# Performance work log

Hardware: AMD Instinct MI355X
Metric: run time of the kernel (lower is better)

The kernel has to match this reference:

```python
import jax, jax.numpy as jnp
import numpy as np

N_NODES = 100000
N_EDGES = 1600000
C = 64          # in = hidden = out channels
L = 3           # num_layers
BN_EPS = 1e-5


def setup_inputs() -> dict:
    key = jax.random.key(0)
    ks = jax.random.split(key, 16)
    x = jax.random.normal(ks[0], (N_NODES, C), dtype=jnp.float32)
    edge_index = jax.random.randint(ks[1], (2, N_EDGES), 0, N_NODES, dtype=jnp.int32)
    s = 1.0 / np.sqrt(C)
    # Stacked per-layer parameters (all layers are C->C).
    # Linear weights stored as [in, out] (i.e. torch weight transposed).
    W1 = jax.random.normal(ks[2], (L, C, C), dtype=jnp.float32) * s
    b1 = jnp.zeros((L, C), dtype=jnp.float32)
    g1 = jnp.ones((L, C), dtype=jnp.float32)    # MLP BN1 gamma
    be1 = jnp.zeros((L, C), dtype=jnp.float32)  # MLP BN1 beta
    W2 = jax.random.normal(ks[3], (L, C, C), dtype=jnp.float32) * s
    b2 = jnp.zeros((L, C), dtype=jnp.float32)
    g2 = jnp.ones((L, C), dtype=jnp.float32)
    be2 = jnp.zeros((L, C), dtype=jnp.float32)
    bn_g = jnp.ones((L, C), dtype=jnp.float32)   # outer per-layer BN gamma
    bn_be = jnp.zeros((L, C), dtype=jnp.float32)
    eps = jnp.zeros((L,), dtype=jnp.float32)     # GIN eps per layer
    return {"x": x, "edge_index": edge_index, "eps": eps,
            "W1": W1, "b1": b1, "g1": g1, "be1": be1,
            "W2": W2, "b2": b2, "g2": g2, "be2": be2,
            "bn_g": bn_g, "bn_be": bn_be}


def _bn(h, g, b):
    # Inference-mode BatchNorm1d with running_mean=0, running_var=1.
    return g * (h * (1.0 / np.sqrt(1.0 + BN_EPS))) + b


def reference(x, edge_index, eps, W1, b1, g1, be1, W2, b2, g2, be2, bn_g, bn_be):
    src, dst = edge_index[0], edge_index[1]
    for i in range(L):
        # GIN message passing: gather source features, scatter-add to targets.
        agg = jax.ops.segment_sum(x[src], dst, num_segments=N_NODES)  # [N, C]
        h = (1.0 + eps[i]) * x + agg
        # 2-layer MLP: Linear -> BN -> ReLU, twice.
        h = jax.nn.relu(_bn(h @ W1[i] + b1[i], g1[i], be1[i]))
        h = jax.nn.relu(_bn(h @ W2[i] + b2[i], g2[i], be2[i]))
        # Outer per-layer BatchNorm.
        x = _bn(h, bn_g[i], bn_be[i])
        if i < L - 1:
            x = jax.nn.relu(x)  # dropout is identity in eval mode
    return x
```

## Files before the change

kernel.cpp:

```cpp
#include <hip/hip_runtime.h>
#include <hip/hip_fp16.h>

#define N_NODES 100000
#define N_EDGES 1600000
#define CH 64
#define NLAYERS 3
#define NBUCKC 98
#define SLABC 18432
#define NFINE (NBUCKC*8)
#define SLABF 2560
#define EPB 4096

typedef _Float16 half8 __attribute__((ext_vector_type(8)));
typedef float floatx4 __attribute__((ext_vector_type(4)));

static __device__ __forceinline__ float4 ld4(const float* p){ return *(const float4*)p; }
static __device__ __forceinline__ unsigned pack2(float a, float b){
  __half2 h = __float22half2_rn(make_float2(a, b));
  return *(unsigned*)&h;
}
static __device__ __forceinline__ half8 ldh8(const unsigned short* p){
  uint4 u = *(const uint4*)p;
  return *(half8*)&u;
}

__global__ __launch_bounds__(256) void binit_kernel(int* __restrict__ btail, int* __restrict__ ftail){
  int i = blockIdx.x*256 + threadIdx.x;
  if (i < NBUCKC) btail[i] = i*SLABC;
  if (i < NFINE)  ftail[i] = i*SLABF;
}

__global__ __launch_bounds__(256) void part1_kernel(const int* __restrict__ src, const int* __restrict__ dst,
                                                    int* __restrict__ btail, int* __restrict__ pairs){
  __shared__ int lpos[NBUCKC];
  __shared__ int gb[NBUCKC];
  int tid = threadIdx.x;
  if (tid < NBUCKC) lpos[tid] = 0;
  __syncthreads();
  int base = blockIdx.x * EPB;
  #pragma unroll 4
  for (int k = 0; k < EPB/256; ++k) {
    int e = base + k*256 + tid;
    if (e < N_EDGES) atomicAdd(&lpos[dst[e] >> 10], 1);
  }
  __syncthreads();
  if (tid < NBUCKC) {
    int cc = lpos[tid];
    gb[tid] = cc ? atomicAdd(&btail[tid], cc) : 0;
    lpos[tid] = 0;
  }
  __syncthreads();
  #pragma unroll 4
  for (int k = 0; k < EPB/256; ++k) {
    int e = base + k*256 + tid;
    if (e < N_EDGES) {
      int d = dst[e];
      int bk = d >> 10;
      int p = atomicAdd(&lpos[bk], 1);
      int idx = gb[bk] + p;
      if (idx < (bk+1)*SLABC)
        pairs[idx] = src[e] | ((d & 1023) << 20);
    }
  }
}

__global__ __launch_bounds__(256) void part2_kernel(const int* __restrict__ pairs, const int* __restrict__ btail,
                                                    int* __restrict__ ftail, int* __restrict__ pairs2){
  __shared__ int cnt[8*32];
  __shared__ int scur[8];
  int tid = threadIdx.x;
  int b = blockIdx.x >> 3;
  int sg = blockIdx.x & 7;
  int e0 = b*SLABC;
  int e1 = btail[b]; int emax = e0 + SLABC; if (e1 > emax) e1 = emax;
  int len = e1 - e0;
  int s0 = e0 + (int)(((long)len * sg) >> 3);
  int s1 = e0 + (int)(((long)len * (sg+1)) >> 3);
  cnt[tid] = 0;
  __syncthreads();
  for (int i = s0 + tid; i < s1; i += 256) {
    int p = pairs[i];
    int fk = ((unsigned)p >> 27);
    atomicAdd(&cnt[(fk<<5) + (tid & 31)], 1);
  }
  __syncthreads();
  if (tid < 8) {
    int tot = 0;
    #pragma unroll
    for (int r = 0; r < 32; ++r) tot += cnt[(tid<<5) + r];
    scur[tid] = tot ? atomicAdd(&ftail[(b<<3) + tid], tot) : 0;
  }
  __syncthreads();
  int lane = tid & 63;
  for (int i = s0 + (tid >> 6)*64; i < s1; i += 256) {
    int my = i + lane;
    bool valid = (my < s1);
    int p = valid ? pairs[my] : 0;
    int fk = valid ? (int)((unsigned)p >> 27) : -1;
    #pragma unroll
    for (int j = 0; j < 8; ++j) {
      unsigned long long mask = __ballot(valid && fk == j);
      if (mask) {
        int leader = __ffsll((long long)mask) - 1;
        int cc = __popcll(mask);
        int basep = 0;
        if (lane == leader) basep = atomicAdd(&scur[j], cc);
        basep = __shfl(basep, leader, 64);
        if (valid && fk == j) {
          int rank = __popcll(mask & ((1ull << lane) - 1ull));
          int pos = basep + rank;
          if (pos < ((b<<3) + j + 1)*SLABF)
            pairs2[pos] = p;
        }
      }
    }
  }
}

__global__ __launch_bounds__(256) void csr_kernel(const int* __restrict__ pairs2, const int* __restrict__ ftail,
                                                  int* __restrict__ offs, int* __restrict__ offe,
                                                  int* __restrict__ srclist){
  __shared__ int c[128];
  __shared__ int s[128];
  __shared__ int cur[128];
  int t = threadIdx.x;
  int f = blockIdx.x;
  int e0 = f*SLABF;
  int e1 = ftail[f]; int emax = e0 + SLABF; if (e1 > emax) e1 = emax;
  if (t < 128) c[t] = 0;
  __syncthreads();
  for (int i = e0 + t; i < e1; i += 256) {
    int p = pairs2[i];
    atomicAdd(&c[((unsigned)p >> 20) & 127], 1);
  }
  __syncthreads();
  int v = (t < 128) ? c[t] : 0;
  if (t < 128) s[t] = v;
  __syncthreads();
  #pragma unroll
  for (int o = 1; o < 128; o <<= 1){
    int u = 0;
    if (t < 128 && t >= o) u = s[t-o];
    __syncthreads();
    if (t < 128) s[t] += u;
    __syncthreads();
  }
  if (t < 128) {
    int excl = s[t] - v;
    cur[t] = excl;
    int n = (f >> 3)*1024 + (f & 7)*128 + t;
    if (n < N_NODES) { offs[n] = e0 + excl; offe[n] = e0 + excl + v; }
  }
  __syncthreads();
  for (int i = e0 + t; i < e1; i += 256) {
    int p = pairs2[i];
    int pos = atomicAdd(&cur[((unsigned)p >> 20) & 127], 1);
    if (pos < SLABF)
      srclist[e0 + pos] = p & 0xFFFFF;
  }
}

__global__ __launch_bounds__(256) void prep_kernel(
    const float* __restrict__ W1, const float* __restrict__ b1,
    const float* __restrict__ g1, const float* __restrict__ be1,
    const float* __restrict__ W2, const float* __restrict__ b2,
    const float* __restrict__ g2, const float* __restrict__ be2,
    const float* __restrict__ bng, const float* __restrict__ bnb,
    _Float16* __restrict__ Wt, float* __restrict__ bf, float* __restrict__ ogb){
  const float s = 0.9999950000374997f;
  int i = blockIdx.x*256 + threadIdx.x;
  if (i < NLAYERS*4096) {
    int l = i >> 12, rem = i & 4095, k = rem >> 6, n = rem & 63;
    int di = n*64 + (((k>>3) ^ (n&7))<<3) + (k&7);
    Wt[l*8192 + di]        = (_Float16)(W1[i] * g1[l*64+n] * s);
    Wt[l*8192 + 4096 + di] = (_Float16)(W2[i] * g2[l*64+n] * s);
  }
  if (i < NLAYERS*64) {
    int l = i >> 6, j = i & 63;
    bf[l*128 + j]      = b1[i]*g1[i]*s + be1[i];
    bf[l*128 + 64 + j] = b2[i]*g2[i]*s + be2[i];
    ogb[i]                 = bng[i]*s;
    ogb[NLAYERS*64 + i]    = bnb[i];
  }
}

__global__ __launch_bounds__(256) void xcvt_kernel(const float* __restrict__ x, unsigned short* __restrict__ xb){
  int i = (blockIdx.x*256 + threadIdx.x)*8;
  if (i < N_NODES*CH) {
    float4 v0 = ld4(x + i), v1 = ld4(x + i + 4);
    uint4 w;
    w.x = pack2(v0.x, v0.y); w.y = pack2(v0.z, v0.w);
    w.z = pack2(v1.x, v1.y); w.w = pack2(v1.z, v1.w);
    *(uint4*)(xb + i) = w;
  }
}

__global__ __launch_bounds__(256, 4) void layer_kernel(const unsigned short* __restrict__ XBin,
                                                    const int* __restrict__ offs, const int* __restrict__ offe,
                                                    const int* __restrict__ srclist,
                                                    const float* __restrict__ eps,
                                                    const _Float16* __restrict__ Wt,
                                                    const float* __restrict__ bf, const float* __restrict__ ogb,
                                                    int layer, float* __restrict__ outf,
                                                    _Float16* __restrict__ outb, int relu_out){
  __shared__ _Float16 HsA[64*64];
  __shared__ _Float16 Wts[64*64];
  int tid = threadIdx.x;
  int b = blockIdx.x;
  const _Float16* Wg = Wt + layer*8192;
  *(uint4*)&Wts[tid*8]       = *(const uint4*)&Wg[tid*8];
  *(uint4*)&Wts[(tid+256)*8] = *(const uint4*)&Wg[(tid+256)*8];

  float ep = 1.0f + eps[layer];
  int kb = tid & 7;
  const unsigned short* xr = XBin + (kb << 3);
  #pragma unroll
  for (int p = 0; p < 2; ++p) {
    int nl = p*32 + (tid >> 3);
    int n = b*64 + nl;
    float r[8] = {0,0,0,0,0,0,0,0};
    if (n < N_NODES) {
      half8 A = (half8)(_Float16)0, B = A, C = A, D = A, E = A, F = A, G = A, H = A;
      int e0 = offs[n], e1 = offe[n];
      int e = e0;
      for (; e+8 <= e1; e += 8) {
        int s0 = srclist[e],   s1 = srclist[e+1], s2 = srclist[e+2], s3 = srclist[e+3];
        int s4 = srclist[e+4], s5 = srclist[e+5], s6 = srclist[e+6], s7 = srclist[e+7];
        half8 u0 = ldh8(xr + (s0<<6));
        half8 u1 = ldh8(xr + (s1<<6));
        half8 u2 = ldh8(xr + (s2<<6));
        half8 u3 = ldh8(xr + (s3<<6));
        half8 u4 = ldh8(xr + (s4<<6));
        half8 u5 = ldh8(xr + (s5<<6));
        half8 u6 = ldh8(xr + (s6<<6));
        half8 u7 = ldh8(xr + (s7<<6));
        A += u0; B += u1; C += u2; D += u3; E += u4; F += u5; G += u6; H += u7;
      }
      for (; e+4 <= e1; e += 4) {
        int s0 = srclist[e], s1 = srclist[e+1], s2 = srclist[e+2], s3 = srclist[e+3];
        half8 u0 = ldh8(xr + (s0<<6));
        half8 u1 = ldh8(xr + (s1<<6));
        half8 u2 = ldh8(xr + (s2<<6));
        half8 u3 = ldh8(xr + (s3<<6));
        A += u0; B += u1; C += u2; D += u3;
      }
      for (; e < e1; ++e) {
        A += ldh8(xr + (srclist[e]<<6));
      }
      half8 S = ((A + B) + (C + D)) + ((E + F) + (G + H));
      half8 sv = ldh8(xr + (n<<6));
      #pragma unroll
      for (int i = 0; i < 8; ++i) r[i] = fmaf(ep, (float)sv[i], (float)S[i]);
    }
    uint4 w;
    w.x = pack2(r[0], r[1]); w.y = pack2(r[2], r[3]);
    w.z = pack2(r[4], r[5]); w.w = pack2(r[6], r[7]);
    *(uint4*)&HsA[nl*64 + ((kb ^ (nl&7))<<3)] = w;
  }
  __syncthreads();

  int lane = tid & 63;
  int wid = tid >> 6;
  int c = lane & 15;
  int q = lane >> 4;
  int mbase = wid*16;
  int ma = mbase + c;

  half8 a0 = *(const half8*)&HsA[ma*64 + (((q)   ^ (ma&7))<<3)];
  half8 a1 = *(const half8*)&HsA[ma*64 + (((4+q) ^ (ma&7))<<3)];

  floatx4 acc[4];
  #pragma unroll
  for (int nt = 0; nt < 4; ++nt) {
    int n = nt*16 + c;
    float bv = bf[layer*128 + n];
    floatx4 Acc = {bv, bv, bv, bv};
    half8 b0 = *(const half8*)&Wts[n*64 + (((q)   ^ (n&7))<<3)];
    half8 b1 = *(const half8*)&Wts[n*64 + (((4+q) ^ (n&7))<<3)];
    Acc = __builtin_amdgcn_mfma_f32_16x16x32_f16(a0, b0, Acc, 0, 0, 0);
    Acc = __builtin_amdgcn_mfma_f32_16x16x32_f16(a1, b1, Acc, 0, 0, 0);
    acc[nt] = Acc;
  }
  __syncthreads();

  #pragma unroll
  for (int nt = 0; nt < 4; ++nt) {
    int n = nt*16 + c;
    #pragma unroll
    for (int r = 0; r < 4; ++r) {
      int m = mbase + q*4 + r;
      float h = acc[nt][r]; h = h > 0.f ? h : 0.f;
      HsA[m*64 + (((n>>3) ^ (m&7))<<3) + (n&7)] = (_Float16)h;
    }
  }
  *(uint4*)&Wts[tid*8]       = *(const uint4*)&Wg[4096 + tid*8];
  *(uint4*)&Wts[(tid+256)*8] = *(const uint4*)&Wg[4096 + (tid+256)*8];
  __syncthreads();

  half8 c0 = *(const half8*)&HsA[ma*64 + (((q)   ^ (ma&7))<<3)];
  half8 c1 = *(const half8*)&HsA[ma*64 + (((4+q) ^ (ma&7))<<3)];
  floatx4 acc2[4];
  #pragma unroll
  for (int nt = 0; nt < 4; ++nt) {
    int n = nt*16 + c;
    float bv = bf[layer*128 + 64 + n];
    floatx4 Acc = {bv, bv, bv, bv};
    half8 b0 = *(const half8*)&Wts[n*64 + (((q)   ^ (n&7))<<3)];
    half8 b1 = *(const half8*)&Wts[n*64 + (((4+q) ^ (n&7))<<3)];
    Acc = __builtin_amdgcn_mfma_f32_16x16x32_f16(c0, b0, Acc, 0, 0, 0);
    Acc = __builtin_amdgcn_mfma_f32_16x16x32_f16(c1, b1, Acc, 0, 0, 0);
    acc2[nt] = Acc;
  }

  #pragma unroll
  for (int nt = 0; nt < 4; ++nt) {
    int n = nt*16 + c;
    float og = ogb[layer*64 + n];
    float ob = ogb[NLAYERS*64 + layer*64 + n];
    #pragma unroll
    for (int r = 0; r < 4; ++r) {
      int m = mbase + q*4 + r;
      int gnode = b*64 + m;
      if (gnode < N_NODES) {
        float h = acc2[nt][r]; h = h > 0.f ? h : 0.f;
        float o = fmaf(og, h, ob);
        if (relu_out) {
          o = o > 0.f ? o : 0.f;
          outb[(size_t)gnode*CH + n] = (_Float16)o;
        } else {
          outf[(size_t)gnode*CH + n] = o;
        }
      }
    }
  }
}

extern "C" void kernel_launch(void* const* d_in, const int* in_sizes, int n_in,
                              void* d_out, int out_size, void* d_ws, size_t ws_size,
                              hipStream_t stream) {
  const float* x0  = (const float*)d_in[0];
  const int*   ei  = (const int*)d_in[1];
  const float* eps = (const float*)d_in[2];
  const float* W1  = (const float*)d_in[3];
  const float* b1  = (const float*)d_in[4];
  const float* g1  = (const float*)d_in[5];
  const float* be1 = (const float*)d_in[6];
  const float* W2  = (const float*)d_in[7];
  const float* b2  = (const float*)d_in[8];
  const float* g2  = (const float*)d_in[9];
  const float* be2 = (const float*)d_in[10];
  const float* bng = (const float*)d_in[11];
  const float* bnb = (const float*)d_in[12];
  const int* src = ei;
  const int* dst = ei + N_EDGES;
  float* OUT = (float*)d_out;

  char* p = (char*)d_ws;
  auto carve = [&](size_t bytes)->char*{ char* r = p; p += (bytes + 255) & ~(size_t)255; return r; };
  int*   offs    = (int*)carve((size_t)N_NODES*sizeof(int));
  int*   offe    = (int*)carve((size_t)N_NODES*sizeof(int));
  int*   btail   = (int*)carve(NBUCKC*sizeof(int));
  int*   ftail   = (int*)carve(NFINE*sizeof(int));
  int*   pairs   = (int*)carve((size_t)NBUCKC*SLABC*sizeof(int));
  int*   pairs2  = (int*)carve((size_t)NFINE*SLABF*sizeof(int));
  int*   srclist = (int*)carve((size_t)NFINE*SLABF*sizeof(int));
  unsigned short* XB0 = (unsigned short*)carve((size_t)N_NODES*CH*2);
  unsigned short* XB1 = (unsigned short*)carve((size_t)N_NODES*CH*2);
  _Float16* Wt   = (_Float16*)carve((size_t)NLAYERS*2*4096*2);
  float* bfb     = (float*)carve((size_t)NLAYERS*2*64*sizeof(float));
  float* ogb     = (float*)carve((size_t)2*NLAYERS*64*sizeof(float));

  const int npart = (N_EDGES + EPB - 1)/EPB;
  binit_kernel<<<(NFINE+255)/256, 256, 0, stream>>>(btail, ftail);
  part1_kernel<<<npart, 256, 0, stream>>>(src, dst, btail, pairs);
  part2_kernel<<<NFINE, 256, 0, stream>>>(pairs, btail, ftail, pairs2);
  csr_kernel<<<NFINE, 256, 0, stream>>>(pairs2, ftail, offs, offe, srclist);
  prep_kernel<<<48, 256, 0, stream>>>(W1,b1,g1,be1,W2,b2,g2,be2,bng,bnb,Wt,bfb,ogb);
  xcvt_kernel<<<(N_NODES*CH/8 + 255)/256, 256, 0, stream>>>(x0, XB0);

  const int nlb = (N_NODES + 63)/64;
  layer_kernel<<<nlb, 256, 0, stream>>>(XB0, offs, offe, srclist, eps, Wt, bfb, ogb, 0, OUT, (_Float16*)XB1, 1);
  layer_kernel<<<nlb, 256, 0, stream>>>(XB1, offs, offe, srclist, eps, Wt, bfb, ogb, 1, OUT, (_Float16*)XB0, 1);
  layer_kernel<<<nlb, 256, 0, stream>>>(XB0, offs, offe, srclist, eps, Wt, bfb, ogb, 2, OUT, (_Float16*)XB1, 0);
}
```

Before: 288.0 us.

## Fold bucket init into prep kernel, cache edges in part1, pipeline gather loads

```diff
diff --git a/kernel.cpp b/kernel.cpp
--- a/kernel.cpp
+++ b/kernel.cpp
@@ -24,12 +24,6 @@
   return *(half8*)&u;
 }
 
-__global__ __launch_bounds__(256) void binit_kernel(int* __restrict__ btail, int* __restrict__ ftail){
-  int i = blockIdx.x*256 + threadIdx.x;
-  if (i < NBUCKC) btail[i] = i*SLABC;
-  if (i < NFINE)  ftail[i] = i*SLABF;
-}
-
 __global__ __launch_bounds__(256) void part1_kernel(const int* __restrict__ src, const int* __restrict__ dst,
                                                     int* __restrict__ btail, int* __restrict__ pairs){
   __shared__ int lpos[NBUCKC];
@@ -38,28 +32,30 @@
   if (tid < NBUCKC) lpos[tid] = 0;
   __syncthreads();
   int base = blockIdx.x * EPB;
-  #pragma unroll 4
+  int es[EPB/256], ed[EPB/256], er[EPB/256];
+  #pragma unroll
   for (int k = 0; k < EPB/256; ++k) {
     int e = base + k*256 + tid;
-    if (e < N_EDGES) atomicAdd(&lpos[dst[e] >> 10], 1);
+    if (e < N_EDGES) {
+      es[k] = src[e];
+      ed[k] = dst[e];
+      er[k] = atomicAdd(&lpos[ed[k] >> 10], 1);
+    }
   }
   __syncthreads();
   if (tid < NBUCKC) {
     int cc = lpos[tid];
     gb[tid] = cc ? atomicAdd(&btail[tid], cc) : 0;
-    lpos[tid] = 0;
-  }
-  __syncthreads();
-  #pragma unroll 4
+  }
+  __syncthreads();
+  #pragma unroll
   for (int k = 0; k < EPB/256; ++k) {
     int e = base + k*256 + tid;
     if (e < N_EDGES) {
-      int d = dst[e];
-      int bk = d >> 10;
-      int p = atomicAdd(&lpos[bk], 1);
-      int idx = gb[bk] + p;
+      int bk = ed[k] >> 10;
+      int idx = gb[bk] + er[k];
       if (idx < (bk+1)*SLABC)
-        pairs[idx] = src[e] | ((d & 1023) << 20);
+        pairs[idx] = es[k] | ((ed[k] & 1023) << 20);
     }
   }
 }
@@ -166,9 +162,12 @@
     const float* __restrict__ W2, const float* __restrict__ b2,
     const float* __restrict__ g2, const float* __restrict__ be2,
     const float* __restrict__ bng, const float* __restrict__ bnb,
-    _Float16* __restrict__ Wt, float* __restrict__ bf, float* __restrict__ ogb){
+    _Float16* __restrict__ Wt, float* __restrict__ bf, float* __restrict__ ogb,
+    int* __restrict__ btail, int* __restrict__ ftail){
   const float s = 0.9999950000374997f;
   int i = blockIdx.x*256 + threadIdx.x;
+  if (i < NBUCKC) btail[i] = i*SLABC;
+  if (i < NFINE)  ftail[i] = i*SLABF;
   if (i < NLAYERS*4096) {
     int l = i >> 12, rem = i & 4095, k = rem >> 6, n = rem & 63;
     int di = n*64 + (((k>>3) ^ (n&7))<<3) + (k&7);
@@ -223,25 +222,38 @@
       half8 A = (half8)(_Float16)0, B = A, C = A, D = A, E = A, F = A, G = A, H = A;
       int e0 = offs[n], e1 = offe[n];
       int e = e0;
-      for (; e+8 <= e1; e += 8) {
-        int s0 = srclist[e],   s1 = srclist[e+1], s2 = srclist[e+2], s3 = srclist[e+3];
-        int s4 = srclist[e+4], s5 = srclist[e+5], s6 = srclist[e+6], s7 = srclist[e+7];
-        half8 u0 = ldh8(xr + (s0<<6));
-        half8 u1 = ldh8(xr + (s1<<6));
-        half8 u2 = ldh8(xr + (s2<<6));
-        half8 u3 = ldh8(xr + (s3<<6));
-        half8 u4 = ldh8(xr + (s4<<6));
-        half8 u5 = ldh8(xr + (s5<<6));
-        half8 u6 = ldh8(xr + (s6<<6));
-        half8 u7 = ldh8(xr + (s7<<6));
-        A += u0; B += u1; C += u2; D += u3; E += u4; F += u5; G += u6; H += u7;
+      if (e + 8 <= e1) {
+        half8 u0 = ldh8(xr + (srclist[e  ]<<6));
+        half8 u1 = ldh8(xr + (srclist[e+1]<<6));
+        half8 u2 = ldh8(xr + (srclist[e+2]<<6));
+        half8 u3 = ldh8(xr + (srclist[e+3]<<6));
+        half8 u4 = ldh8(xr + (srclist[e+4]<<6));
+        half8 u5 = ldh8(xr + (srclist[e+5]<<6));
+        half8 u6 = ldh8(xr + (srclist[e+6]<<6));
+        half8 u7 = ldh8(xr + (srclist[e+7]<<6));
+        e += 8;
+        for (; e + 8 <= e1; e += 8) {
+          half8 v0 = ldh8(xr + (srclist[e  ]<<6));
+          half8 v1 = ldh8(xr + (srclist[e+1]<<6));
+          half8 v2 = ldh8(xr + (srclist[e+2]<<6));
+          half8 v3 = ldh8(xr + (srclist[e+3]<<6));
+          half8 v4 = ldh8(xr + (srclist[e+4]<<6));
+          half8 v5 = ldh8(xr + (srclist[e+5]<<6));
+          half8 v6 = ldh8(xr + (srclist[e+6]<<6));
+          half8 v7 = ldh8(xr + (srclist[e+7]<<6));
+          A += u0; B += u1; C += u2; D += u3;
+          E += u4; F += u5; G += u6; H += u7;
+          u0 = v0; u1 = v1; u2 = v2; u3 = v3;
+          u4 = v4; u5 = v5; u6 = v6; u7 = v7;
+        }
+        A += u0; B += u1; C += u2; D += u3;
+        E += u4; F += u5; G += u6; H += u7;
       }
       for (; e+4 <= e1; e += 4) {
-        int s0 = srclist[e], s1 = srclist[e+1], s2 = srclist[e+2], s3 = srclist[e+3];
-        half8 u0 = ldh8(xr + (s0<<6));
-        half8 u1 = ldh8(xr + (s1<<6));
-        half8 u2 = ldh8(xr + (s2<<6));
-        half8 u3 = ldh8(xr + (s3<<6));
+        half8 u0 = ldh8(xr + (srclist[e  ]<<6));
+        half8 u1 = ldh8(xr + (srclist[e+1]<<6));
+        half8 u2 = ldh8(xr + (srclist[e+2]<<6));
+        half8 u3 = ldh8(xr + (srclist[e+3]<<6));
         A += u0; B += u1; C += u2; D += u3;
       }
       for (; e < e1; ++e) {
@@ -371,11 +383,10 @@
   float* ogb     = (float*)carve((size_t)2*NLAYERS*64*sizeof(float));
 
   const int npart = (N_EDGES + EPB - 1)/EPB;
-  binit_kernel<<<(NFINE+255)/256, 256, 0, stream>>>(btail, ftail);
+  prep_kernel<<<48, 256, 0, stream>>>(W1,b1,g1,be1,W2,b2,g2,be2,bng,bnb,Wt,bfb,ogb,btail,ftail);
   part1_kernel<<<npart, 256, 0, stream>>>(src, dst, btail, pairs);
   part2_kernel<<<NFINE, 256, 0, stream>>>(pairs, btail, ftail, pairs2);
   csr_kernel<<<NFINE, 256, 0, stream>>>(pairs2, ftail, offs, offe, srclist);
-  prep_kernel<<<48, 256, 0, stream>>>(W1,b1,g1,be1,W2,b2,g2,be2,bng,bnb,Wt,bfb,ogb);
   xcvt_kernel<<<(N_NODES*CH/8 + 255)/256, 256, 0, stream>>>(x0, XB0);
 
   const int nlb = (N_NODES + 63)/64;
```

Result: no change. 285.1 us (-1.0%).
